# Kernel tuning notes

Measured on AMD Instinct MI355X. Metric: run time of the kernel, lower is better.

Reference implementation:

```python
import jax, jax.numpy as jnp
import numpy as np

# dims
H = 1024          # hidden_size
E = 2048          # d_inner = 2*H
NH = 32           # nheads = E/64
P = 64            # headdim
N = 128           # d_state
G = 1             # ngroups
K = 4             # d_conv
Q = 128           # SSD chunk length
FF = 4096         # intermediate_size
EPS = 1e-6        # rms_norm_eps
NEPS = 1e-5       # mamba gated-norm eps
CONV_DIM = E + 2 * G * N            # 2304
D_IN = 2 * E + 2 * G * N + NH       # 4384


def rmsnorm(x, w, eps):
    v = jnp.mean(x.astype(jnp.float32) ** 2, axis=-1, keepdims=True)
    return (x.astype(jnp.float32) * jax.lax.rsqrt(v + eps)).astype(x.dtype) * w


def segsum(x):
    # x: [..., T] -> [..., T, T] with out[i,j] = sum_{j<k<=i} x[k], -inf above diag
    T = x.shape[-1]
    cs = jnp.cumsum(x, axis=-1)
    s = cs[..., :, None] - cs[..., None, :]
    mask = jnp.tril(jnp.ones((T, T), dtype=bool))
    return jnp.where(mask, s, -jnp.inf)


def ssd(x, dt, A_log, B, C):
    # x:[b,l,nh,p], dt:[b,l,nh], B,C:[b,l,N] (ngroups=1, shared over heads)
    b, l, nh, p = x.shape
    A = -jnp.exp(A_log)                      # [nh]
    dA = dt * A                              # [b,l,nh]
    xd = x * dt[..., None]                   # discretized input
    c = l // Q
    xd = xd.reshape(b, c, Q, nh, p)
    dAc = dA.reshape(b, c, Q, nh).transpose(0, 3, 1, 2)   # [b,h,c,q]
    Bc = B.reshape(b, c, Q, N)
    Cc = C.reshape(b, c, Q, N)
    A_cs = jnp.cumsum(dAc, axis=-1)                        # [b,h,c,q]
    Lm = jnp.exp(segsum(dAc))                              # [b,h,c,q,q]
    # intra-chunk (diagonal blocks)
    Y_diag = jnp.einsum('bcqn,bcsn,bhcqs,bcshp->bcqhp', Cc, Bc, Lm, xd)
    # per-chunk final states
    decay_states = jnp.exp(A_cs[..., -1:] - A_cs)          # [b,h,c,q]
    states = jnp.einsum('bcqn,bhcq,bcqhp->bchpn', Bc, decay_states, xd)
    # inter-chunk recurrence (initial state = 0)
    A_last = jnp.pad(A_cs[..., -1], ((0, 0), (0, 0), (1, 0)))   # [b,h,c+1]
    decay_chunk = jnp.exp(segsum(A_last))                       # [b,h,c+1,c+1]
    states = jnp.concatenate([jnp.zeros_like(states[:, :1]), states], axis=1)
    new_states = jnp.einsum('bhzc,bchpn->bzhpn', decay_chunk, states)[:, :-1]
    Y_off = jnp.einsum('bcqn,bchpn,bhcq->bcqhp', Cc, new_states, jnp.exp(A_cs))
    return (Y_diag + Y_off).reshape(b, l, nh, p)


def mamba2(h, w_in, w_conv, b_conv, dt_bias, A_log, D, w_mnorm, w_out):
    b, l, _ = h.shape
    zxbcdt = h @ w_in.T                         # [b,l,D_IN]
    z, xBC, dt = jnp.split(zxbcdt, [E, E + CONV_DIM], axis=-1)
    # causal depthwise conv (kernel K) over channels of xBC
    pad = jnp.pad(xBC, ((0, 0), (K - 1, 0), (0, 0)))
    xBC = sum(pad[:, k:k + l, :] * w_conv[:, k] for k in range(K)) + b_conv
    xBC = jax.nn.silu(xBC)
    x, B, C = jnp.split(xBC, [E, E + G * N], axis=-1)
    dt = jax.nn.softplus(dt + dt_bias)          # [b,l,NH]
    xh = x.reshape(b, l, NH, P)
    y = ssd(xh, dt, A_log, B, C)
    y = y + D[None, None, :, None] * xh         # per-head skip
    y = y.reshape(b, l, E)
    y = rmsnorm(y * jax.nn.silu(z), w_mnorm, NEPS)   # gated RMSNorm
    return y @ w_out.T


def setup_inputs() -> dict:
    key = jax.random.key(0)
    ks = jax.random.split(key, 12)
    dt0 = jax.random.uniform(ks[0], (NH,), minval=0.001, maxval=0.1)
    dt_bias = dt0 + jnp.log(-jnp.expm1(-dt0))   # inverse softplus
    return {
        'hidden_states': jax.random.normal(ks[1], (2, 2048, H), dtype=jnp.float32),
        'w_ln1': jnp.ones((H,), jnp.float32),
        'w_in': 0.02 * jax.random.normal(ks[2], (D_IN, H), dtype=jnp.float32),
        'w_conv': 0.1 * jax.random.normal(ks[3], (CONV_DIM, K), dtype=jnp.float32),
        'b_conv': jnp.zeros((CONV_DIM,), jnp.float32),
        'dt_bias': dt_bias,
        'A_log': jnp.log(jax.random.uniform(ks[4], (NH,), minval=1.0, maxval=16.0)),
        'D': jnp.ones((NH,), jnp.float32),
        'w_mnorm': jnp.ones((E,), jnp.float32),
        'w_out': 0.02 * jax.random.normal(ks[5], (H, E), dtype=jnp.float32),
        'w_ln2': jnp.ones((H,), jnp.float32),
        'w_gate': 0.02 * jax.random.normal(ks[6], (FF, H), dtype=jnp.float32),
        'w_up': 0.02 * jax.random.normal(ks[7], (FF, H), dtype=jnp.float32),
        'w_down': 0.02 * jax.random.normal(ks[8], (H, FF), dtype=jnp.float32),
    }


def reference(hidden_states, w_ln1, w_in, w_conv, b_conv, dt_bias, A_log, D,
              w_mnorm, w_out, w_ln2, w_gate, w_up, w_down):
    residual = hidden_states
    h = rmsnorm(hidden_states, w_ln1, EPS)
    h = mamba2(h, w_in, w_conv, b_conv, dt_bias, A_log, D, w_mnorm, w_out)
    hidden = residual + h
    residual = hidden
    h = rmsnorm(hidden, w_ln2, EPS)
    h = (jax.nn.silu(h @ w_gate.T) * (h @ w_up.T)) @ w_down.T
    return residual + h
```

## Files before the change

### kernel.cpp

```cpp
#include <hip/hip_runtime.h>

#define DEV static __device__ __forceinline__

typedef short bf16x8 __attribute__((ext_vector_type(8)));
typedef float floatx4 __attribute__((ext_vector_type(4)));
typedef unsigned short ushort4v __attribute__((ext_vector_type(4)));
typedef unsigned short ushort8v __attribute__((ext_vector_type(8)));

DEV unsigned short f32_bf16(float f) {
  unsigned int u = __builtin_bit_cast(unsigned int, f);
  u = u + 0x7fffu + ((u >> 16) & 1u);
  return (unsigned short)(u >> 16);
}
DEV float bf2f(unsigned short u) {
  unsigned int v = ((unsigned int)u) << 16;
  return __builtin_bit_cast(float, v);
}
DEV float sigmoidf_(float x) { return 1.0f / (1.0f + __expf(-x)); }
DEV float siluf_(float x) { return x * sigmoidf_(x); }

#define GLD_LDS16(g, l)                                                              \
  __builtin_amdgcn_global_load_lds((const __attribute__((address_space(1))) void*)(g), \
                                   (__attribute__((address_space(3))) void*)(l), 16, 0, 0)

template <int MODE>
__global__ __launch_bounds__(256) void gemm128(
    const unsigned short* __restrict__ A, const unsigned short* __restrict__ B,
    void* __restrict__ Cv, const unsigned short* __restrict__ other,
    int K, int lda, int ldb, int ldc, long long bsA, long long bsB, long long bsC) {
  __shared__ unsigned short As[128 * 32];
  __shared__ unsigned short Bs[128 * 32];
  A += (long long)blockIdx.z * bsA;
  B += (long long)blockIdx.z * bsB;
  const long long coff = (long long)blockIdx.z * bsC;
  const int tid = threadIdx.x;
  const int w = tid >> 6, lane = tid & 63;

  const int nbx = gridDim.x, nby = gridDim.y;
  const int GM = 4;
  int bid = blockIdx.y * nbx + blockIdx.x;
  int gid = bid / (GM * nbx);
  int rem = bid - gid * (GM * nbx);
  int gsz = min(GM, nby - gid * GM);
  int mtile = gid * GM + rem % gsz;
  int ntile = rem / gsz;
  const int m0 = mtile << 7, n0 = ntile << 7;

  const int srow = lane >> 2;
  const int schunk = ((lane & 3) ^ (srow & 3)) * 8;
  const unsigned short* ag0 = A + (long long)(m0 + w * 32 + srow) * lda + schunk;
  const unsigned short* ag1 = ag0 + (long long)16 * lda;
  const unsigned short* bg0 = B + (long long)(n0 + w * 32 + srow) * ldb + schunk;
  const unsigned short* bg1 = bg0 + (long long)16 * ldb;
  unsigned short* al0 = As + (w * 32) * 32 + lane * 8;
  unsigned short* al1 = As + (w * 32 + 16) * 32 + lane * 8;
  unsigned short* bl0 = Bs + (w * 32) * 32 + lane * 8;
  unsigned short* bl1 = Bs + (w * 32 + 16) * 32 + lane * 8;

  const int wr = (w >> 1) << 6, wc = (w & 1) << 6;
  const int fr = lane & 15;
  const int slot = (((lane >> 4) ^ (fr & 3))) << 3;

  floatx4 acc[4][4];
#pragma unroll
  for (int i = 0; i < 4; ++i)
#pragma unroll
    for (int j = 0; j < 4; ++j) acc[i][j] = (floatx4){0.f, 0.f, 0.f, 0.f};

  for (int k0 = 0; k0 < K; k0 += 32) {
    __syncthreads();
    GLD_LDS16(ag0 + k0, al0);
    GLD_LDS16(ag1 + k0, al1);
    GLD_LDS16(bg0 + k0, bl0);
    GLD_LDS16(bg1 + k0, bl1);
    __syncthreads();
    bf16x8 af[4], bf_[4];
#pragma unroll
    for (int i = 0; i < 4; ++i)
      af[i] = *(const bf16x8*)(As + (wr + i * 16 + fr) * 32 + slot);
#pragma unroll
    for (int j = 0; j < 4; ++j)
      bf_[j] = *(const bf16x8*)(Bs + (wc + j * 16 + fr) * 32 + slot);
#pragma unroll
    for (int i = 0; i < 4; ++i)
#pragma unroll
      for (int j = 0; j < 4; ++j)
        acc[i][j] = __builtin_amdgcn_mfma_f32_16x16x32_bf16(af[i], bf_[j], acc[i][j], 0, 0, 0);
  }

  const int r0 = (lane >> 4) << 2;
#pragma unroll
  for (int i = 0; i < 4; ++i) {
#pragma unroll
    for (int j = 0; j < 4; ++j) {
      long long base = (long long)(m0 + wr + i * 16 + r0) * ldc + (n0 + wc + j * 16 + fr);
#pragma unroll
      for (int r = 0; r < 4; ++r) {
        long long idx = coff + base + (long long)r * ldc;
        float v = acc[i][j][r];
        if constexpr (MODE == 0) {
          ((float*)Cv)[idx] = v;
        } else if constexpr (MODE == 1) {
          ((unsigned short*)Cv)[idx] = f32_bf16(v);
        } else {
          ((unsigned short*)Cv)[idx] = f32_bf16(siluf_(v) * bf2f(other[idx]));
        }
      }
    }
  }
}

template <int WM>
__global__ __launch_bounds__(256) void gemm_small_nt(
    const unsigned short* __restrict__ A, const unsigned short* __restrict__ B,
    float* __restrict__ C, int M, int N, int K, int lda, int ldb, int ldc) {
  const int w = threadIdx.x >> 6;
  const int lane = threadIdx.x & 63;
  const int lm = lane & 15;
  const int ko = (lane >> 4) << 3;
  const int bn0 = blockIdx.x << 6;
  const int m_base = blockIdx.y * (WM * 64) + w * (WM * 16);

  const unsigned short* arow[WM];
#pragma unroll
  for (int i = 0; i < WM; ++i) arow[i] = A + (long long)(m_base + i * 16 + lm) * lda + ko;
  int nv = (N - bn0) >> 4;
  nv = nv > 4 ? 4 : nv;
  const unsigned short* brow[4];
#pragma unroll
  for (int j = 0; j < 4; ++j) {
    int nr = bn0 + j * 16 + lm;
    brow[j] = B + (long long)(j < nv ? nr : 0) * ldb + ko;
  }
  floatx4 acc[WM][4];
#pragma unroll
  for (int i = 0; i < WM; ++i)
#pragma unroll
    for (int j = 0; j < 4; ++j) acc[i][j] = (floatx4){0.f, 0.f, 0.f, 0.f};
  for (int k0 = 0; k0 < K; k0 += 32) {
    bf16x8 a[WM];
#pragma unroll
    for (int i = 0; i < WM; ++i) a[i] = *(const bf16x8*)(arow[i] + k0);
#pragma unroll
    for (int j = 0; j < 4; ++j) {
      if (j < nv) {
        bf16x8 b = *(const bf16x8*)(brow[j] + k0);
#pragma unroll
        for (int i = 0; i < WM; ++i)
          acc[i][j] = __builtin_amdgcn_mfma_f32_16x16x32_bf16(a[i], b, acc[i][j], 0, 0, 0);
      }
    }
  }
  const int r0 = (lane >> 4) << 2;
#pragma unroll
  for (int i = 0; i < WM; ++i)
#pragma unroll
    for (int j = 0; j < 4; ++j)
      if (j < nv) {
        int col = bn0 + j * 16 + lm;
        long long base = (long long)(m_base + i * 16 + r0) * ldc + col;
#pragma unroll
        for (int r = 0; r < 4; ++r) C[base + (long long)r * ldc] = acc[i][j][r];
      }
}

__global__ __launch_bounds__(256) void f32_to_bf16_k(const float* __restrict__ src,
                                                     unsigned short* __restrict__ dst,
                                                     long long n4) {
  long long i = (long long)blockIdx.x * 256 + threadIdx.x;
  if (i < n4) {
    float4 v = ((const float4*)src)[i];
    ushort4v o = {f32_bf16(v.x), f32_bf16(v.y), f32_bf16(v.z), f32_bf16(v.w)};
    ((ushort4v*)dst)[i] = o;
  }
}

__global__ __launch_bounds__(256) void zero_out_k(float* __restrict__ o, long long n) {
  long long i = (long long)blockIdx.x * 256 + threadIdx.x;
  if (i < n) o[i] = 0.f;
}

__global__ __launch_bounds__(256) void rmsnorm1024_bf16_k(const float* __restrict__ x,
                                                          const float* __restrict__ w,
                                                          unsigned short* __restrict__ out,
                                                          float eps) {
  long long row = blockIdx.x;
  int t = threadIdx.x;
  float4 v = ((const float4*)(x + row * 1024))[t];
  float ss = v.x * v.x + v.y * v.y + v.z * v.z + v.w * v.w;
  __shared__ float red[4];
#pragma unroll
  for (int o = 32; o > 0; o >>= 1) ss += __shfl_down(ss, o, 64);
  if ((t & 63) == 0) red[t >> 6] = ss;
  __syncthreads();
  float tot = red[0] + red[1] + red[2] + red[3];
  float sc = rsqrtf(tot * (1.0f / 1024.0f) + eps);
  float4 wv = ((const float4*)w)[t];
  ushort4v o = {f32_bf16(v.x * sc * wv.x), f32_bf16(v.y * sc * wv.y),
                f32_bf16(v.z * sc * wv.z), f32_bf16(v.w * sc * wv.w)};
  ((ushort4v*)(out + row * 1024))[t] = o;
}

__global__ __launch_bounds__(256) void add_rmsnorm_k(const float* __restrict__ hs,
                                                     const float* __restrict__ parts,
                                                     long long pstride, int np,
                                                     const float* __restrict__ w,
                                                     float* __restrict__ mh,
                                                     unsigned short* __restrict__ h2, float eps) {
  long long row = blockIdx.x;
  int t = threadIdx.x;
  float4 v = ((const float4*)(hs + row * 1024))[t];
  for (int p = 0; p < np; ++p) {
    float4 u = ((const float4*)(parts + p * pstride + row * 1024))[t];
    v.x += u.x;
    v.y += u.y;
    v.z += u.z;
    v.w += u.w;
  }
  ((float4*)(mh + row * 1024))[t] = v;
  float ss = v.x * v.x + v.y * v.y + v.z * v.z + v.w * v.w;
  __shared__ float red[4];
#pragma unroll
  for (int o = 32; o > 0; o >>= 1) ss += __shfl_down(ss, o, 64);
  if ((t & 63) == 0) red[t >> 6] = ss;
  __syncthreads();
  float tot = red[0] + red[1] + red[2] + red[3];
  float sc = rsqrtf(tot * (1.0f / 1024.0f) + eps);
  float4 wv = ((const float4*)w)[t];
  ushort4v o = {f32_bf16(v.x * sc * wv.x), f32_bf16(v.y * sc * wv.y),
                f32_bf16(v.z * sc * wv.z), f32_bf16(v.w * sc * wv.w)};
  ((ushort4v*)(h2 + row * 1024))[t] = o;
}

__global__ __launch_bounds__(256) void addn_f32_k(const float* __restrict__ a,
                                                  const float* __restrict__ parts,
                                                  long long pstride, int np,
                                                  float* __restrict__ o, long long n4) {
  long long i = (long long)blockIdx.x * 256 + threadIdx.x;
  if (i < n4) {
    float4 x = ((const float4*)a)[i];
    for (int p = 0; p < np; ++p) {
      float4 u = ((const float4*)(parts + p * pstride))[i];
      x.x += u.x;
      x.y += u.y;
      x.z += u.z;
      x.w += u.w;
    }
    ((float4*)o)[i] = x;
  }
}

__global__ __launch_bounds__(256) void gated_rmsnorm2048_k(const unsigned short* __restrict__ y,
                                                           const unsigned short* __restrict__ z,
                                                           const float* __restrict__ w,
                                                           unsigned short* __restrict__ out,
                                                           float eps) {
  long long row = blockIdx.x;
  int t = threadIdx.x;
  ushort8v yv = ((const ushort8v*)(y + row * 2048))[t];
  ushort8v zv = ((const ushort8v*)(z + row * 2048))[t];
  float g[8];
  float ss = 0.f;
#pragma unroll
  for (int j = 0; j < 8; ++j) {
    g[j] = bf2f(yv[j]) * siluf_(bf2f(zv[j]));
    ss += g[j] * g[j];
  }
  __shared__ float red[4];
#pragma unroll
  for (int o = 32; o > 0; o >>= 1) ss += __shfl_down(ss, o, 64);
  if ((t & 63) == 0) red[t >> 6] = ss;
  __syncthreads();
  float tot = red[0] + red[1] + red[2] + red[3];
  float sc = rsqrtf(tot * (1.0f / 2048.0f) + eps);
  float ww[8];
  *(float4*)&ww[0] = ((const float4*)w)[2 * t];
  *(float4*)&ww[4] = ((const float4*)w)[2 * t + 1];
  ushort8v o;
#pragma unroll
  for (int j = 0; j < 8; ++j) o[j] = f32_bf16(g[j] * sc * ww[j]);
  ((ushort8v*)(out + row * 2048))[t] = o;
}

__global__ __launch_bounds__(256) void conv_silu_k(const unsigned short* __restrict__ xraw,
                                                   const float* __restrict__ wconv,
                                                   const float* __restrict__ bconv,
                                                   unsigned short* __restrict__ xBC) {
  int m = blockIdx.x;
  int l = m & 2047;
  for (int cb = threadIdx.x; cb < 288; cb += 256) {
    int ch0 = cb << 3;
    float acc[8];
    float4 bc0 = ((const float4*)bconv)[cb * 2];
    float4 bc1 = ((const float4*)bconv)[cb * 2 + 1];
    acc[0] = bc0.x; acc[1] = bc0.y; acc[2] = bc0.z; acc[3] = bc0.w;
    acc[4] = bc1.x; acc[5] = bc1.y; acc[6] = bc1.z; acc[7] = bc1.w;
    float4 wv[8];
#pragma unroll
    for (int j = 0; j < 8; ++j) wv[j] = ((const float4*)wconv)[ch0 + j];
#pragma unroll
    for (int k = 0; k < 4; ++k) {
      int lk = l + k - 3;
      if (lk >= 0) {
        ushort8v xv = *(const ushort8v*)(xraw + (long long)(m + k - 3) * 2304 + ch0);
        acc[0] += bf2f(xv[0]) * ((const float*)&wv[0])[k];
        acc[1] += bf2f(xv[1]) * ((const float*)&wv[1])[k];
        acc[2] += bf2f(xv[2]) * ((const float*)&wv[2])[k];
        acc[3] += bf2f(xv[3]) * ((const float*)&wv[3])[k];
        acc[4] += bf2f(xv[4]) * ((const float*)&wv[4])[k];
        acc[5] += bf2f(xv[5]) * ((const float*)&wv[5])[k];
        acc[6] += bf2f(xv[6]) * ((const float*)&wv[6])[k];
        acc[7] += bf2f(xv[7]) * ((const float*)&wv[7])[k];
      }
    }
    ushort8v o;
#pragma unroll
    for (int j = 0; j < 8; ++j) o[j] = f32_bf16(siluf_(acc[j]));
    *(ushort8v*)(xBC + (long long)m * 2304 + ch0) = o;
  }
}

__global__ __launch_bounds__(256) void dt_softplus_k(const float* __restrict__ dtraw,
                                                     const float* __restrict__ dt_bias,
                                                     float* __restrict__ dt_s) {
  int i = blockIdx.x * 256 + threadIdx.x;
  float xv = dtraw[i] + dt_bias[i & 31];
  dt_s[i] = xv > 20.f ? xv : log1pf(expf(xv));
}

__global__ __launch_bounds__(128) void dA_cumsum_k(const float* __restrict__ dt_s,
                                                   const float* __restrict__ A_log,
                                                   float* __restrict__ dA_cs) {
  int bi = blockIdx.x;
  int c = bi & 15, h = (bi >> 4) & 31, b = bi >> 9;
  int q = threadIdx.x;
  float A = -expf(A_log[h]);
  float v = dt_s[((long long)(b * 2048 + c * 128 + q)) * 32 + h] * A;
  __shared__ float sbuf[128];
  sbuf[q] = v;
  __syncthreads();
  for (int off = 1; off < 128; off <<= 1) {
    float tv = (q >= off) ? sbuf[q - off] : 0.f;
    __syncthreads();
    sbuf[q] += tv;
    __syncthreads();
  }
  dA_cs[(long long)bi * 128 + q] = sbuf[q];
}

__global__ __launch_bounds__(256) void ssd_diag_states_k(
    const unsigned short* __restrict__ xBC, const float* __restrict__ dt_s,
    const float* __restrict__ dA_cs, const unsigned short* __restrict__ G,
    unsigned short* __restrict__ y, unsigned short* __restrict__ states) {
  __shared__ unsigned short Mz[128 * 136];
  __shared__ unsigned short xdT[64 * 136];
  __shared__ float Acs[128];
  __shared__ float wdec[128];
  const int bx = blockIdx.x;
  const int h = bx & 31, c = (bx >> 5) & 15, b = bx >> 9;
  const int t = threadIdx.x;
  const int w = t >> 6, lane = t & 63, fr = lane & 15, hi = lane >> 4;
  const long long rowbase = (long long)b * 2048 + c * 128;
  const long long abase = ((long long)((b * 32 + h) * 16 + c)) << 7;

  if (t < 128) {
    float a = dA_cs[abase + t];
    Acs[t] = a;
    wdec[t] = __expf(dA_cs[abase + 127] - a);
  }
  {
    int s = t >> 1, p0 = (t & 1) * 32;
    float dtv = dt_s[(rowbase + s) * 32 + h];
    const ushort8v* xv = (const ushort8v*)(xBC + (rowbase + s) * 2304 + h * 64 + p0);
#pragma unroll
    for (int i = 0; i < 4; ++i) {
      ushort8v vv = xv[i];
#pragma unroll
      for (int j = 0; j < 8; ++j) xdT[(p0 + i * 8 + j) * 136 + s] = f32_bf16(bf2f(vv[j]) * dtv);
    }
  }
  __syncthreads();
  {
    int q = t >> 1, s0 = (t & 1) * 64;
    float aq = Acs[q];
    const ushort8v* gv =
        (const ushort8v*)(G + (((long long)(b * 16 + c)) * 128 + q) * 128 + s0);
#pragma unroll
    for (int i = 0; i < 8; ++i) {
      ushort8v gg = gv[i];
#pragma unroll
      for (int j = 0; j < 8; ++j) {
        int s = s0 + i * 8 + j;
        float m = (s <= q) ? bf2f(gg[j]) * __expf(aq - Acs[s]) : 0.f;
        Mz[q * 136 + s] = f32_bf16(m);
      }
    }
  }
  __syncthreads();
  const int q0 = w << 5;
  {
    floatx4 acc[2][4];
#pragma unroll
    for (int i = 0; i < 2; ++i)
#pragma unroll
      for (int j = 0; j < 4; ++j) acc[i][j] = (floatx4){0.f, 0.f, 0.f, 0.f};
#pragma unroll
    for (int k0 = 0; k0 < 128; k0 += 32) {
      int kk = k0 + hi * 8;
      bf16x8 a0 = *(const bf16x8*)(Mz + (q0 + fr) * 136 + kk);
      bf16x8 a1 = *(const bf16x8*)(Mz + (q0 + 16 + fr) * 136 + kk);
      bf16x8 bf_[4];
#pragma unroll
      for (int j = 0; j < 4; ++j) bf_[j] = *(const bf16x8*)(xdT + (j * 16 + fr) * 136 + kk);
#pragma unroll
      for (int j = 0; j < 4; ++j) {
        acc[0][j] = __builtin_amdgcn_mfma_f32_16x16x32_bf16(a0, bf_[j], acc[0][j], 0, 0, 0);
        acc[1][j] = __builtin_amdgcn_mfma_f32_16x16x32_bf16(a1, bf_[j], acc[1][j], 0, 0, 0);
      }
    }
#pragma unroll
    for (int i = 0; i < 2; ++i)
#pragma unroll
      for (int r = 0; r < 4; ++r) {
        int q = q0 + i * 16 + hi * 4 + r;
        unsigned short* yrow = y + (rowbase + q) * 2048 + h * 64;
#pragma unroll
        for (int j = 0; j < 4; ++j) yrow[j * 16 + fr] = f32_bf16(acc[i][j][r]);
      }
  }
  __syncthreads();
  {
    int s = t >> 1, n0 = (t & 1) * 64;
    float wd = wdec[s];
    const ushort8v* bv = (const ushort8v*)(xBC + (rowbase + s) * 2304 + 2048 + n0);
#pragma unroll
    for (int i = 0; i < 8; ++i) {
      ushort8v bb = bv[i];
#pragma unroll
      for (int j = 0; j < 8; ++j) Mz[(n0 + i * 8 + j) * 136 + s] = f32_bf16(bf2f(bb[j]) * wd);
    }
  }
  __syncthreads();
  {
    floatx4 acc[2][4];
#pragma unroll
    for (int i = 0; i < 2; ++i)
#pragma unroll
      for (int j = 0; j < 4; ++j) acc[i][j] = (floatx4){0.f, 0.f, 0.f, 0.f};
#pragma unroll
    for (int k0 = 0; k0 < 128; k0 += 32) {
      int kk = k0 + hi * 8;
      bf16x8 a0 = *(const bf16x8*)(Mz + (q0 + fr) * 136 + kk);
      bf16x8 a1 = *(const bf16x8*)(Mz + (q0 + 16 + fr) * 136 + kk);
      bf16x8 bf_[4];
#pragma unroll
      for (int j = 0; j < 4; ++j) bf_[j] = *(const bf16x8*)(xdT + (j * 16 + fr) * 136 + kk);
#pragma unroll
      for (int j = 0; j < 4; ++j) {
        acc[0][j] = __builtin_amdgcn_mfma_f32_16x16x32_bf16(a0, bf_[j], acc[0][j], 0, 0, 0);
        acc[1][j] = __builtin_amdgcn_mfma_f32_16x16x32_bf16(a1, bf_[j], acc[1][j], 0, 0, 0);
      }
    }
    unsigned short* st = states + (long long)bx * 8192;
#pragma unroll
    for (int i = 0; i < 2; ++i)
#pragma unroll
      for (int j = 0; j < 4; ++j) {
        int p = j * 16 + fr;
        int n = q0 + i * 16 + hi * 4;
        ushort4v o;
#pragma unroll
        for (int r = 0; r < 4; ++r) o[r] = f32_bf16(acc[i][j][r]);
        *(ushort4v*)(st + p * 128 + n) = o;
      }
  }
}

__global__ __launch_bounds__(256) void ssd_scan_k(const float* __restrict__ dA_cs,
                                                  unsigned short* __restrict__ states) {
  int h = blockIdx.x & 31, b = blockIdx.x >> 5;
  int t = threadIdx.x;
  float carry[32];
#pragma unroll
  for (int i = 0; i < 32; ++i) carry[i] = 0.f;
  for (int c = 0; c < 16; ++c) {
    long long base = ((long long)((b * 16 + c) * 32 + h)) * 8192;
    float dec = __expf(dA_cs[(((long long)((b * 32 + h) * 16 + c)) << 7) + 127]);
#pragma unroll
    for (int i = 0; i < 32; ++i) {
      long long idx = base + t + i * 256;
      float local = bf2f(states[idx]);
      states[idx] = f32_bf16(carry[i]);
      carry[i] = dec * carry[i] + local;
    }
  }
}

__global__ __launch_bounds__(256) void ssd_off_k(const unsigned short* __restrict__ xBC,
                                                 const float* __restrict__ dA_cs,
                                                 const unsigned short* __restrict__ states,
                                                 const float* __restrict__ Dvec,
                                                 unsigned short* __restrict__ y) {
  __shared__ float eA[128];
  const int bx = blockIdx.x;
  const int h = bx & 31, c = (bx >> 5) & 15, b = bx >> 9;
  const int t = threadIdx.x;
  const int w = t >> 6, lane = t & 63, fr = lane & 15, hi = lane >> 4;
  const long long rowbase = (long long)b * 2048 + c * 128;
  const long long abase = ((long long)((b * 32 + h) * 16 + c)) << 7;
  if (t < 128) eA[t] = __expf(dA_cs[abase + t]);
  __syncthreads();

  const unsigned short* st = states + (long long)bx * 8192;
  const int q0 = w << 5;
  floatx4 acc[2][4];
#pragma unroll
  for (int i = 0; i < 2; ++i)
#pragma unroll
    for (int j = 0; j < 4; ++j) acc[i][j] = (floatx4){0.f, 0.f, 0.f, 0.f};

#pragma unroll
  for (int k0 = 0; k0 < 128; k0 += 32) {
    int kk = k0 + hi * 8;
    bf16x8 a0 = *(const bf16x8*)(xBC + (rowbase + q0 + fr) * 2304 + 2176 + kk);
    bf16x8 a1 = *(const bf16x8*)(xBC + (rowbase + q0 + 16 + fr) * 2304 + 2176 + kk);
    bf16x8 bf_[4];
#pragma unroll
    for (int j = 0; j < 4; ++j) bf_[j] = *(const bf16x8*)(st + (j * 16 + fr) * 128 + kk);
#pragma unroll
    for (int j = 0; j < 4; ++j) {
      acc[0][j] = __builtin_amdgcn_mfma_f32_16x16x32_bf16(a0, bf_[j], acc[0][j], 0, 0, 0);
      acc[1][j] = __builtin_amdgcn_mfma_f32_16x16x32_bf16(a1, bf_[j], acc[1][j], 0, 0, 0);
    }
  }

  float Dh = Dvec[h];
#pragma unroll
  for (int i = 0; i < 2; ++i) {
#pragma unroll
    for (int r = 0; r < 4; ++r) {
      int q = q0 + i * 16 + hi * 4 + r;
      float e = eA[q];
      const unsigned short* xrow = xBC + (rowbase + q) * 2304 + h * 64;
      unsigned short* yrow = y + (rowbase + q) * 2048 + h * 64;
#pragma unroll
      for (int j = 0; j < 4; ++j) {
        int p = j * 16 + fr;
        float v = bf2f(yrow[p]) + e * acc[i][j][r] + Dh * bf2f(xrow[p]);
        yrow[p] = f32_bf16(v);
      }
    }
  }
}

extern "C" void kernel_launch(void* const* d_in, const int* in_sizes, int n_in, void* d_out,
                              int out_size, void* d_ws, size_t ws_size, hipStream_t stream) {
  const float* hs = (const float*)d_in[0];
  const float* w_ln1 = (const float*)d_in[1];
  const float* w_in = (const float*)d_in[2];
  const float* w_conv = (const float*)d_in[3];
  const float* b_conv = (const float*)d_in[4];
  const float* dt_bias = (const float*)d_in[5];
  const float* A_log = (const float*)d_in[6];
  const float* Dvec = (const float*)d_in[7];
  const float* w_mnorm = (const float*)d_in[8];
  const float* w_out = (const float*)d_in[9];
  const float* w_ln2 = (const float*)d_in[10];
  const float* w_gate = (const float*)d_in[11];
  const float* w_up = (const float*)d_in[12];
  const float* w_down = (const float*)d_in[13];
  float* out = (float*)d_out;
  const int M = 4096;

  char* ws = (char*)d_ws;
  const size_t R0 = 0;
  const size_t R1 = 33554432;
  const size_t R1b = R1 + 33554432;
  const size_t R2 = 71303168;
  const size_t R3 = 90177536;
  const size_t R4 = 107544576;
  const size_t W0 = 108068864;
  const size_t NEED = 133234688;

  if (ws_size < NEED) {
    hipLaunchKernelGGL(zero_out_k, dim3((out_size + 255) / 256), dim3(256), 0, stream, out,
                       (long long)out_size);
    return;
  }

  unsigned short* z = (unsigned short*)(ws + R0);
  unsigned short* act = (unsigned short*)(ws + R0);
  float* oproj_parts = (float*)(ws + R0);
  unsigned short* xraw = (unsigned short*)(ws + R1);
  unsigned short* states = (unsigned short*)(ws + R1);
  unsigned short* ybuf = (unsigned short*)(ws + R1 + 16777216);
  unsigned short* upo = (unsigned short*)(ws + R1);
  float* down_parts = (float*)(ws + R1);
  unsigned short* wbf_out = (unsigned short*)(ws + R1b);
  unsigned short* xBC = (unsigned short*)(ws + R2);
  unsigned short* ygn = (unsigned short*)(ws + R2);
  unsigned short* h2 = (unsigned short*)(ws + R2);
  unsigned short* hnorm = (unsigned short*)(ws + R3);
  unsigned short* wbf_in = (unsigned short*)(ws + R3 + 8388608);
  float* dt_s = (float*)(ws + R3);
  float* dA_cs = (float*)(ws + R3 + 524288);
  unsigned short* Gbuf = (unsigned short*)(ws + R3 + 1048576);
  float* mh = (float*)(ws + R3);
  float* dtraw = (float*)(ws + R4);
  unsigned short* wbf_gate = (unsigned short*)(ws + W0);
  unsigned short* wbf_up = (unsigned short*)(ws + W0 + 8388608);
  unsigned short* wbf_down = (unsigned short*)(ws + W0 + 16777216);

  hipLaunchKernelGGL(rmsnorm1024_bf16_k, dim3(M), dim3(256), 0, stream, hs, w_ln1, hnorm, 1e-6f);
  hipLaunchKernelGGL(f32_to_bf16_k, dim3(4384), dim3(256), 0, stream, w_in, wbf_in, 1122304LL);
  hipLaunchKernelGGL(f32_to_bf16_k, dim3(4096), dim3(256), 0, stream, w_gate, wbf_gate, 1048576LL);
  hipLaunchKernelGGL(f32_to_bf16_k, dim3(4096), dim3(256), 0, stream, w_up, wbf_up, 1048576LL);
  hipLaunchKernelGGL(f32_to_bf16_k, dim3(4096), dim3(256), 0, stream, w_down, wbf_down, 1048576LL);
  hipLaunchKernelGGL((gemm128<1>), dim3(16, 32, 1), dim3(256), 0, stream, hnorm, wbf_in, (void*)z,
                     (const unsigned short*)nullptr, 1024, 1024, 1024, 2048, 0LL, 0LL, 0LL);
  hipLaunchKernelGGL((gemm128<1>), dim3(18, 32, 1), dim3(256), 0, stream, hnorm,
                     wbf_in + 2048 * 1024, (void*)xraw, (const unsigned short*)nullptr, 1024, 1024,
                     1024, 2304, 0LL, 0LL, 0LL);
  hipLaunchKernelGGL((gemm_small_nt<4>), dim3(1, 16, 1), dim3(256), 0, stream, hnorm,
                     wbf_in + 4352 * 1024, dtraw, M, 32, 1024, 1024, 1024, 32);
  hipLaunchKernelGGL(conv_silu_k, dim3(M), dim3(256), 0, stream, xraw, w_conv, b_conv, xBC);
  hipLaunchKernelGGL(f32_to_bf16_k, dim3(2048), dim3(256), 0, stream, w_out, wbf_out, 524288LL);
  hipLaunchKernelGGL(dt_softplus_k, dim3(512), dim3(256), 0, stream, dtraw, dt_bias, dt_s);
  hipLaunchKernelGGL(dA_cumsum_k, dim3(1024), dim3(128), 0, stream, dt_s, A_log, dA_cs);
  hipLaunchKernelGGL((gemm128<1>), dim3(1, 1, 32), dim3(256), 0, stream, xBC + 2176, xBC + 2048,
                     (void*)Gbuf, (const unsigned short*)nullptr, 128, 2304, 2304, 128, 294912LL,
                     294912LL, 16384LL);
  hipLaunchKernelGGL(ssd_diag_states_k, dim3(1024), dim3(256), 0, stream, xBC, dt_s, dA_cs, Gbuf,
                     ybuf, states);
  hipLaunchKernelGGL(ssd_scan_k, dim3(64), dim3(256), 0, stream, dA_cs, states);
  hipLaunchKernelGGL(ssd_off_k, dim3(1024), dim3(256), 0, stream, xBC, dA_cs, states, Dvec, ybuf);
  hipLaunchKernelGGL(gated_rmsnorm2048_k, dim3(M), dim3(256), 0, stream, ybuf, z, w_mnorm, ygn,
                     1e-5f);
  hipLaunchKernelGGL((gemm128<0>), dim3(8, 32, 4), dim3(256), 0, stream, ygn, wbf_out,
                     (void*)oproj_parts, (const unsigned short*)nullptr, 512, 2048, 2048, 1024,
                     512LL, 512LL, 4194304LL);
  hipLaunchKernelGGL(add_rmsnorm_k, dim3(M), dim3(256), 0, stream, hs, oproj_parts, 4194304LL, 4,
                     w_ln2, mh, h2, 1e-6f);
  hipLaunchKernelGGL((gemm128<1>), dim3(32, 32, 1), dim3(256), 0, stream, h2, wbf_up, (void*)upo,
                     (const unsigned short*)nullptr, 1024, 1024, 1024, 4096, 0LL, 0LL, 0LL);
  hipLaunchKernelGGL((gemm128<2>), dim3(32, 32, 1), dim3(256), 0, stream, h2, wbf_gate, (void*)act,
                     upo, 1024, 1024, 1024, 4096, 0LL, 0LL, 0LL);
  hipLaunchKernelGGL((gemm128<0>), dim3(8, 32, 2), dim3(256), 0, stream, act, wbf_down,
                     (void*)down_parts, (const unsigned short*)nullptr, 2048, 4096, 4096, 1024,
                     2048LL, 2048LL, 4194304LL);
  hipLaunchKernelGGL(addn_f32_k, dim3(4096), dim3(256), 0, stream, mh, down_parts, 4194304LL, 2,
                     out, 1048576LL);
}
```

Baseline: 626.6 us.

## Fuse gate and up GEMMs into a dual-accumulator kernel and add XCD-aware block remap

```diff
diff --git a/kernel.cpp b/kernel.cpp
--- a/kernel.cpp
+++ b/kernel.cpp
@@ -18,6 +18,12 @@
 }
 DEV float sigmoidf_(float x) { return 1.0f / (1.0f + __expf(-x)); }
 DEV float siluf_(float x) { return x * sigmoidf_(x); }
+
+DEV int xcd_map(int bid, int nwg) {
+  int q = nwg >> 3, r = nwg & 7;
+  int xcd = bid & 7, idx = bid >> 3;
+  return (xcd < r ? xcd * (q + 1) : r * (q + 1) + (xcd - r) * q) + idx;
+}
 
 #define GLD_LDS16(g, l)                                                              \
   __builtin_amdgcn_global_load_lds((const __attribute__((address_space(1))) void*)(g), \
@@ -38,7 +44,7 @@
 
   const int nbx = gridDim.x, nby = gridDim.y;
   const int GM = 4;
-  int bid = blockIdx.y * nbx + blockIdx.x;
+  int bid = xcd_map(blockIdx.y * nbx + blockIdx.x, nbx * nby);
   int gid = bid / (GM * nbx);
   int rem = bid - gid * (GM * nbx);
   int gsz = min(GM, nby - gid * GM);
@@ -105,6 +111,96 @@
         } else {
           ((unsigned short*)Cv)[idx] = f32_bf16(siluf_(v) * bf2f(other[idx]));
         }
+      }
+    }
+  }
+}
+
+__global__ __launch_bounds__(256) void gemm128_dual(
+    const unsigned short* __restrict__ A, const unsigned short* __restrict__ Bg,
+    const unsigned short* __restrict__ Bu, unsigned short* __restrict__ C,
+    int K, int lda, int ldb, int ldc) {
+  __shared__ unsigned short As[128 * 32];
+  __shared__ unsigned short Bgs[128 * 32];
+  __shared__ unsigned short Bus[128 * 32];
+  const int tid = threadIdx.x;
+  const int w = tid >> 6, lane = tid & 63;
+
+  const int nbx = gridDim.x, nby = gridDim.y;
+  const int GM = 4;
+  int bid = xcd_map(blockIdx.y * nbx + blockIdx.x, nbx * nby);
+  int gid = bid / (GM * nbx);
+  int rem = bid - gid * (GM * nbx);
+  int gsz = min(GM, nby - gid * GM);
+  int mtile = gid * GM + rem % gsz;
+  int ntile = rem / gsz;
+  const int m0 = mtile << 7, n0 = ntile << 7;
+
+  const int srow = lane >> 2;
+  const int schunk = ((lane & 3) ^ (srow & 3)) * 8;
+  const unsigned short* ag0 = A + (long long)(m0 + w * 32 + srow) * lda + schunk;
+  const unsigned short* ag1 = ag0 + (long long)16 * lda;
+  const unsigned short* gg0 = Bg + (long long)(n0 + w * 32 + srow) * ldb + schunk;
+  const unsigned short* gg1 = gg0 + (long long)16 * ldb;
+  const unsigned short* ug0 = Bu + (long long)(n0 + w * 32 + srow) * ldb + schunk;
+  const unsigned short* ug1 = ug0 + (long long)16 * ldb;
+  unsigned short* al0 = As + (w * 32) * 32 + lane * 8;
+  unsigned short* al1 = As + (w * 32 + 16) * 32 + lane * 8;
+  unsigned short* gl0 = Bgs + (w * 32) * 32 + lane * 8;
+  unsigned short* gl1 = Bgs + (w * 32 + 16) * 32 + lane * 8;
+  unsigned short* ul0 = Bus + (w * 32) * 32 + lane * 8;
+  unsigned short* ul1 = Bus + (w * 32 + 16) * 32 + lane * 8;
+
+  const int wr = (w >> 1) << 6, wc = (w & 1) << 6;
+  const int fr = lane & 15;
+  const int slot = (((lane >> 4) ^ (fr & 3))) << 3;
+
+  floatx4 accg[4][4], accu[4][4];
+#pragma unroll
+  for (int i = 0; i < 4; ++i)
+#pragma unroll
+    for (int j = 0; j < 4; ++j) {
+      accg[i][j] = (floatx4){0.f, 0.f, 0.f, 0.f};
+      accu[i][j] = (floatx4){0.f, 0.f, 0.f, 0.f};
+    }
+
+  for (int k0 = 0; k0 < K; k0 += 32) {
+    __syncthreads();
+    GLD_LDS16(ag0 + k0, al0);
+    GLD_LDS16(ag1 + k0, al1);
+    GLD_LDS16(gg0 + k0, gl0);
+    GLD_LDS16(gg1 + k0, gl1);
+    GLD_LDS16(ug0 + k0, ul0);
+    GLD_LDS16(ug1 + k0, ul1);
+    __syncthreads();
+    bf16x8 af[4], gf[4], uf[4];
+#pragma unroll
+    for (int i = 0; i < 4; ++i)
+      af[i] = *(const bf16x8*)(As + (wr + i * 16 + fr) * 32 + slot);
+#pragma unroll
+    for (int j = 0; j < 4; ++j) {
+      gf[j] = *(const bf16x8*)(Bgs + (wc + j * 16 + fr) * 32 + slot);
+      uf[j] = *(const bf16x8*)(Bus + (wc + j * 16 + fr) * 32 + slot);
+    }
+#pragma unroll
+    for (int i = 0; i < 4; ++i)
+#pragma unroll
+      for (int j = 0; j < 4; ++j) {
+        accg[i][j] = __builtin_amdgcn_mfma_f32_16x16x32_bf16(af[i], gf[j], accg[i][j], 0, 0, 0);
+        accu[i][j] = __builtin_amdgcn_mfma_f32_16x16x32_bf16(af[i], uf[j], accu[i][j], 0, 0, 0);
+      }
+  }
+
+  const int r0 = (lane >> 4) << 2;
+#pragma unroll
+  for (int i = 0; i < 4; ++i) {
+#pragma unroll
+    for (int j = 0; j < 4; ++j) {
+      long long base = (long long)(m0 + wr + i * 16 + r0) * ldc + (n0 + wc + j * 16 + fr);
+#pragma unroll
+      for (int r = 0; r < 4; ++r) {
+        float v = siluf_(accg[i][j][r]) * accu[i][j][r];
+        ((unsigned short*)C)[base + (long long)r * ldc] = f32_bf16(v);
       }
     }
   }
@@ -594,7 +690,6 @@
   unsigned short* xraw = (unsigned short*)(ws + R1);
   unsigned short* states = (unsigned short*)(ws + R1);
   unsigned short* ybuf = (unsigned short*)(ws + R1 + 16777216);
-  unsigned short* upo = (unsigned short*)(ws + R1);
   float* down_parts = (float*)(ws + R1);
   unsigned short* wbf_out = (unsigned short*)(ws + R1b);
   unsigned short* xBC = (unsigned short*)(ws + R2);
@@ -641,10 +736,8 @@
                      512LL, 512LL, 4194304LL);
   hipLaunchKernelGGL(add_rmsnorm_k, dim3(M), dim3(256), 0, stream, hs, oproj_parts, 4194304LL, 4,
                      w_ln2, mh, h2, 1e-6f);
-  hipLaunchKernelGGL((gemm128<1>), dim3(32, 32, 1), dim3(256), 0, stream, h2, wbf_up, (void*)upo,
-                     (const unsigned short*)nullptr, 1024, 1024, 1024, 4096, 0LL, 0LL, 0LL);
-  hipLaunchKernelGGL((gemm128<2>), dim3(32, 32, 1), dim3(256), 0, stream, h2, wbf_gate, (void*)act,
-                     upo, 1024, 1024, 1024, 4096, 0LL, 0LL, 0LL);
+  hipLaunchKernelGGL(gemm128_dual, dim3(32, 32, 1), dim3(256), 0, stream, h2, wbf_gate, wbf_up,
+                     act, 1024, 1024, 1024, 4096);
   hipLaunchKernelGGL((gemm128<0>), dim3(8, 32, 2), dim3(256), 0, stream, act, wbf_down,
                      (void*)down_parts, (const unsigned short*)nullptr, 2048, 4096, 4096, 1024,
                      2048LL, 2048LL, 4194304LL);
```

Result: slower. 675.6 us (+7.8%).

## Double-buffer GEMM LDS loads and split SSD scan across more blocks

Applied to the files above, without the earlier changes.

```diff
diff --git a/kernel.cpp b/kernel.cpp
--- a/kernel.cpp
+++ b/kernel.cpp
@@ -28,8 +28,8 @@
     const unsigned short* __restrict__ A, const unsigned short* __restrict__ B,
     void* __restrict__ Cv, const unsigned short* __restrict__ other,
     int K, int lda, int ldb, int ldc, long long bsA, long long bsB, long long bsC) {
-  __shared__ unsigned short As[128 * 32];
-  __shared__ unsigned short Bs[128 * 32];
+  __shared__ unsigned short As[2 * 128 * 32];
+  __shared__ unsigned short Bs[2 * 128 * 32];
   A += (long long)blockIdx.z * bsA;
   B += (long long)blockIdx.z * bsB;
   const long long coff = (long long)blockIdx.z * bsC;
@@ -52,10 +52,15 @@
   const unsigned short* ag1 = ag0 + (long long)16 * lda;
   const unsigned short* bg0 = B + (long long)(n0 + w * 32 + srow) * ldb + schunk;
   const unsigned short* bg1 = bg0 + (long long)16 * ldb;
-  unsigned short* al0 = As + (w * 32) * 32 + lane * 8;
-  unsigned short* al1 = As + (w * 32 + 16) * 32 + lane * 8;
-  unsigned short* bl0 = Bs + (w * 32) * 32 + lane * 8;
-  unsigned short* bl1 = Bs + (w * 32 + 16) * 32 + lane * 8;
+  const int s_off = w * 1024 + lane * 8;
+
+#define STAGE128(buf, k0)                              \
+  do {                                                 \
+    GLD_LDS16(ag0 + (k0), As + (buf) * 4096 + s_off);  \
+    GLD_LDS16(ag1 + (k0), As + (buf) * 4096 + s_off + 512); \
+    GLD_LDS16(bg0 + (k0), Bs + (buf) * 4096 + s_off);  \
+    GLD_LDS16(bg1 + (k0), Bs + (buf) * 4096 + s_off + 512); \
+  } while (0)
 
   const int wr = (w >> 1) << 6, wc = (w & 1) << 6;
   const int fr = lane & 15;
@@ -67,26 +72,37 @@
 #pragma unroll
     for (int j = 0; j < 4; ++j) acc[i][j] = (floatx4){0.f, 0.f, 0.f, 0.f};
 
-  for (int k0 = 0; k0 < K; k0 += 32) {
-    __syncthreads();
-    GLD_LDS16(ag0 + k0, al0);
-    GLD_LDS16(ag1 + k0, al1);
-    GLD_LDS16(bg0 + k0, bl0);
-    GLD_LDS16(bg1 + k0, bl1);
-    __syncthreads();
+  const int nsteps = K >> 5;
+  STAGE128(0, 0);
+  if (nsteps > 1) STAGE128(1, 32);
+
+  for (int t = 0; t < nsteps; ++t) {
+    if (t < nsteps - 1) {
+      asm volatile("s_waitcnt vmcnt(4)" ::: "memory");
+    } else {
+      asm volatile("s_waitcnt vmcnt(0)" ::: "memory");
+    }
+    __builtin_amdgcn_s_barrier();
+    __builtin_amdgcn_sched_barrier(0);
+    const unsigned short* Ab = As + (t & 1) * 4096;
+    const unsigned short* Bb = Bs + (t & 1) * 4096;
     bf16x8 af[4], bf_[4];
 #pragma unroll
     for (int i = 0; i < 4; ++i)
-      af[i] = *(const bf16x8*)(As + (wr + i * 16 + fr) * 32 + slot);
+      af[i] = *(const bf16x8*)(Ab + (wr + i * 16 + fr) * 32 + slot);
 #pragma unroll
     for (int j = 0; j < 4; ++j)
-      bf_[j] = *(const bf16x8*)(Bs + (wc + j * 16 + fr) * 32 + slot);
+      bf_[j] = *(const bf16x8*)(Bb + (wc + j * 16 + fr) * 32 + slot);
 #pragma unroll
     for (int i = 0; i < 4; ++i)
 #pragma unroll
       for (int j = 0; j < 4; ++j)
         acc[i][j] = __builtin_amdgcn_mfma_f32_16x16x32_bf16(af[i], bf_[j], acc[i][j], 0, 0, 0);
-  }
+    __builtin_amdgcn_sched_barrier(0);
+    __builtin_amdgcn_s_barrier();
+    if (t + 2 < nsteps) STAGE128(t & 1, (t + 2) * 32);
+  }
+#undef STAGE128
 
   const int r0 = (lane >> 4) << 2;
 #pragma unroll
@@ -478,17 +494,20 @@
 
 __global__ __launch_bounds__(256) void ssd_scan_k(const float* __restrict__ dA_cs,
                                                   unsigned short* __restrict__ states) {
-  int h = blockIdx.x & 31, b = blockIdx.x >> 5;
+  int seg = blockIdx.x & 7;
+  int h = (blockIdx.x >> 3) & 31;
+  int b = blockIdx.x >> 8;
   int t = threadIdx.x;
-  float carry[32];
-#pragma unroll
-  for (int i = 0; i < 32; ++i) carry[i] = 0.f;
+  int e0 = seg * 1024 + t;
+  float carry[4];
+#pragma unroll
+  for (int i = 0; i < 4; ++i) carry[i] = 0.f;
   for (int c = 0; c < 16; ++c) {
     long long base = ((long long)((b * 16 + c) * 32 + h)) * 8192;
     float dec = __expf(dA_cs[(((long long)((b * 32 + h) * 16 + c)) << 7) + 127]);
 #pragma unroll
-    for (int i = 0; i < 32; ++i) {
-      long long idx = base + t + i * 256;
+    for (int i = 0; i < 4; ++i) {
+      long long idx = base + e0 + i * 256;
       float local = bf2f(states[idx]);
       states[idx] = f32_bf16(carry[i]);
       carry[i] = dec * carry[i] + local;
@@ -632,7 +651,7 @@
                      294912LL, 16384LL);
   hipLaunchKernelGGL(ssd_diag_states_k, dim3(1024), dim3(256), 0, stream, xBC, dt_s, dA_cs, Gbuf,
                      ybuf, states);
-  hipLaunchKernelGGL(ssd_scan_k, dim3(64), dim3(256), 0, stream, dA_cs, states);
+  hipLaunchKernelGGL(ssd_scan_k, dim3(512), dim3(256), 0, stream, dA_cs, states);
   hipLaunchKernelGGL(ssd_off_k, dim3(1024), dim3(256), 0, stream, xBC, dA_cs, states, Dvec, ybuf);
   hipLaunchKernelGGL(gated_rmsnorm2048_k, dim3(M), dim3(256), 0, stream, ybuf, z, w_mnorm, ygn,
                      1e-5f);
```

Measured after the change: 573.5 us. -8.5%, faster.
